# Kernel optimization log

Hardware: AMD Instinct MI355X
Metric: run time of the kernel (lower is better)

Reference implementation:

```python
import jax, jax.numpy as jnp
import numpy as np

IOU_THRESH = 0.5


def _iou_xcycwh(a, b):
    # a: (A,4) center-format anchors, b: (M,4) center-format gt boxes -> (A,M)
    ax1, ay1 = a[:, 0] - a[:, 2] * 0.5, a[:, 1] - a[:, 3] * 0.5
    ax2, ay2 = a[:, 0] + a[:, 2] * 0.5, a[:, 1] + a[:, 3] * 0.5
    bx1, by1 = b[:, 0] - b[:, 2] * 0.5, b[:, 1] - b[:, 3] * 0.5
    bx2, by2 = b[:, 0] + b[:, 2] * 0.5, b[:, 1] + b[:, 3] * 0.5
    iw = jnp.clip(jnp.minimum(ax2[:, None], bx2[None, :]) - jnp.maximum(ax1[:, None], bx1[None, :]), 0.0)
    ih = jnp.clip(jnp.minimum(ay2[:, None], by2[None, :]) - jnp.maximum(ay1[:, None], by1[None, :]), 0.0)
    inter = iw * ih
    area_a = (a[:, 2] * a[:, 3])[:, None]
    area_b = (b[:, 2] * b[:, 3])[None, :]
    return inter / (area_a + area_b - inter)


def _per_image(cls_pred, reg_pred, ann, anchors, num_classes):
    # cls_pred: (A,C) probs in (0,1); reg_pred: (A,5); ann: (M,5) [x,y,w,h,cls]; anchors: (A,4)
    dt = cls_pred.dtype
    valid = ann[:, 4] != -1
    # top-left -> center (matches in-place += w/2, h/2 in torch)
    boxes = jnp.stack([ann[:, 0] + ann[:, 2] * 0.5, ann[:, 1] + ann[:, 3] * 0.5, ann[:, 2], ann[:, 3]], axis=-1)
    ious = _iou_xcycwh(anchors, boxes)                       # (A,M)
    ious = jnp.where(valid[None, :], ious, -jnp.inf)
    ious_max = ious.max(axis=1)
    ious_argmax = ious.argmax(axis=1)
    pos = ious_max >= IOU_THRESH                             # (A,)
    posf = pos.astype(dt)
    npos = pos.sum()
    denom = jnp.maximum(npos, 1).astype(dt)                  # clamp(num_positive_anchors, min=1)
    assigned = jnp.concatenate([boxes, ann[:, 4:5]], axis=-1)[ious_argmax]  # (A,5)
    gt_cls = jax.nn.one_hot(assigned[:, 4].astype(jnp.int32), num_classes, dtype=dt) * posf[:, None]
    bce = -(gt_cls * jnp.log(cls_pred) + (1.0 - gt_cls) * jnp.log(1.0 - cls_pred))
    cls_loss = (bce * posf[:, None]).sum() / denom
    gt_w = jnp.maximum(assigned[:, 2], 1.0)
    gt_h = jnp.maximum(assigned[:, 3], 1.0)
    sig_tx_gt = jax.nn.sigmoid(assigned[:, 0] - anchors[:, 0])
    sig_ty_gt = jax.nn.sigmoid(assigned[:, 1] - anchors[:, 1])
    tw_gt = jnp.log(gt_w / anchors[:, 2])
    th_gt = jnp.log(gt_h / anchors[:, 3])

    def mse(p, t):  # MSELoss over positive anchors = masked sum / npos
        return (posf * (p - t) ** 2).sum() / denom

    reg = (mse(jax.nn.sigmoid(reg_pred[:, 0]), sig_tx_gt)
           + mse(jax.nn.sigmoid(reg_pred[:, 1]), sig_ty_gt)
           + mse(reg_pred[:, 2], tw_gt)
           + mse(reg_pred[:, 3], th_gt)
           + mse(reg_pred[:, 4], jnp.ones_like(reg_pred[:, 4])))
    reg_loss = jnp.where(npos > 0, reg / denom, jnp.zeros((), dt))
    has_valid = valid.any()
    cls_loss = jnp.where(has_valid, cls_loss, jnp.zeros((), dt))
    return cls_loss, reg_loss


def reference(predictions, bbox_annotations, anchors, input_dim, num_classes, num_anchors, grid_size):
    B = predictions.shape[0]
    cls = predictions[..., 5:].reshape(B, -1, num_classes)   # (B,A,C)
    reg = predictions[..., :5].reshape(B, -1, 5)             # (B,A,5)
    anc = anchors.reshape(-1, 4)                             # (A,4)
    cls_l, reg_l = jax.vmap(lambda c, r, a: _per_image(c, r, a, anc, num_classes))(cls, reg, bbox_annotations)
    return cls_l.mean(keepdims=True), reg_l.mean(keepdims=True)


def setup_inputs() -> dict:
    key = jax.random.key(0)
    k1, k2, k3, k4 = jax.random.split(key, 4)
    B, NA, G, C, M, INPUT = 16, 3, 76, 80, 32, 608
    stride = INPUT / G
    # predictions: probabilities/pre-sigmoid values in (0.01, 0.99) (raw log requires p in (0,1))
    u = jax.random.uniform(k1, (B, NA, G, G, C + 5), dtype=jnp.float32)
    predictions = 0.01 + 0.98 * u
    # anchors: grid-cell centers in pixels + 3 per-cell anchor sizes
    xs = (jnp.arange(G, dtype=jnp.float32) + 0.5) * stride
    cyg, cxg = jnp.meshgrid(xs, xs, indexing='ij')
    sizes = jnp.array([[12.0, 16.0], [24.0, 32.0], [48.0, 40.0]], dtype=jnp.float32)
    anchors = jnp.stack([
        jnp.broadcast_to(cxg, (NA, G, G)),
        jnp.broadcast_to(cyg, (NA, G, G)),
        jnp.broadcast_to(sizes[:, 0][:, None, None], (NA, G, G)),
        jnp.broadcast_to(sizes[:, 1][:, None, None], (NA, G, G))], axis=-1)
    # annotations: top-left x,y + w,h in pixels + class id; last 8 boxes padded with cls=-1
    wh = jax.random.uniform(k2, (B, M, 2), minval=8.0, maxval=64.0)
    xy = jax.random.uniform(k3, (B, M, 2), minval=0.0, maxval=INPUT - 64.0)
    cls_id = jax.random.randint(k4, (B, M, 1), 0, C).astype(jnp.float32)
    valid = (jnp.arange(M) < 24)[None, :, None]
    ann = jnp.concatenate([xy, wh, jnp.where(valid, cls_id, -1.0)], axis=-1)
    return {"predictions": predictions, "bbox_annotations": ann, "anchors": anchors,
            "input_dim": INPUT, "num_classes": C, "num_anchors": NA, "grid_size": G}
```

## Files before the change

kernel.cpp:

```cpp
#include <hip/hip_runtime.h>
#include <math.h>


#define NCLS 85
#define CVAL 80
#define BLK  256

__device__ __forceinline__ float sigm(float x) {
    return 1.0f / (1.0f + expf(-x));
}

__global__ void __launch_bounds__(BLK)
yolo_match_kernel(const float* __restrict__ pred,
                  const float* __restrict__ ann,
                  const float* __restrict__ anc,
                  float* __restrict__ partial,
                  int A, int M)
{
    const int b = blockIdx.y;
    const int a = blockIdx.x * BLK + threadIdx.x;

    __shared__ float s_bx1[64], s_by1[64], s_bx2[64], s_by2[64];
    __shared__ float s_bcx[64], s_bcy[64], s_bw[64], s_bh[64], s_area[64];
    __shared__ int   s_cls[64];

    if (threadIdx.x < (unsigned)M) {
        const int m = threadIdx.x;
        const float* r = ann + ((long long)b * M + m) * 5;
        const float x = r[0], y = r[1], w = r[2], h = r[3], c = r[4];
        const float cx = x + 0.5f * w;
        const float cy = y + 0.5f * h;
        s_bcx[m] = cx; s_bcy[m] = cy; s_bw[m] = w; s_bh[m] = h;
        s_bx1[m] = cx - 0.5f * w; s_by1[m] = cy - 0.5f * h;
        s_bx2[m] = cx + 0.5f * w; s_by2[m] = cy + 0.5f * h;
        s_area[m] = w * h;
        s_cls[m] = (c != -1.0f) ? (int)c : -1;
    }
    __syncthreads();

    float cls_sum = 0.0f, reg_sq = 0.0f, np = 0.0f;

    if (a < A) {
        const float4 av = ((const float4*)anc)[a];
        const float acx = av.x, acy = av.y, aw = av.z, ah = av.w;
        const float ax1 = acx - 0.5f * aw, ay1 = acy - 0.5f * ah;
        const float ax2 = acx + 0.5f * aw, ay2 = acy + 0.5f * ah;
        const float aarea = aw * ah;

        float best = -INFINITY;
        int bm = 0;
        for (int m = 0; m < M; ++m) {
            float iw = fminf(ax2, s_bx2[m]) - fmaxf(ax1, s_bx1[m]);
            float ih = fminf(ay2, s_by2[m]) - fmaxf(ay1, s_by1[m]);
            iw = fmaxf(iw, 0.0f);
            ih = fmaxf(ih, 0.0f);
            const float inter = iw * ih;
            float iou = inter / (aarea + s_area[m] - inter);
            if (s_cls[m] < 0) iou = -INFINITY;
            if (iou > best) { best = iou; bm = m; }
        }

        if (best >= 0.5f) {
            np = 1.0f;
            const float bcx = s_bcx[bm], bcy = s_bcy[bm];
            const float bw = s_bw[bm], bh = s_bh[bm];
            const int k = s_cls[bm];

            const float* row = pred + ((long long)b * A + a) * NCLS;

            const float r0 = row[0], r1 = row[1], r2 = row[2], r3 = row[3], r4 = row[4];
            const float e0 = sigm(r0) - sigm(bcx - acx);
            const float e1 = sigm(r1) - sigm(bcy - acy);
            const float e2 = r2 - logf(fmaxf(bw, 1.0f) / aw);
            const float e3 = r3 - logf(fmaxf(bh, 1.0f) / ah);
            const float e4 = r4 - 1.0f;
            reg_sq = e0*e0 + e1*e1 + e2*e2 + e3*e3 + e4*e4;

            for (int c = 0; c < CVAL; ++c) {
                const float p = row[5 + c];
                cls_sum += (c == k) ? -logf(p) : -logf(1.0f - p);
            }
        }
    }

    for (int off = 32; off > 0; off >>= 1) {
        cls_sum += __shfl_down(cls_sum, off);
        reg_sq  += __shfl_down(reg_sq,  off);
        np      += __shfl_down(np,      off);
    }
    __shared__ float s_red[4][3];
    const int wave = threadIdx.x >> 6;
    const int lane = threadIdx.x & 63;
    if (lane == 0) {
        s_red[wave][0] = cls_sum;
        s_red[wave][1] = reg_sq;
        s_red[wave][2] = np;
    }
    __syncthreads();
    if (threadIdx.x == 0) {
        float c = 0.0f, r = 0.0f, n = 0.0f;
        for (int w = 0; w < 4; ++w) { c += s_red[w][0]; r += s_red[w][1]; n += s_red[w][2]; }
        float* dst = partial + ((long long)b * gridDim.x + blockIdx.x) * 3;
        dst[0] = c; dst[1] = r; dst[2] = n;
    }
}

__global__ void __launch_bounds__(256)
yolo_finalize_kernel(const float* __restrict__ partial,
                     float* __restrict__ out, int B, int P)
{
    const int t = threadIdx.x;
    const int b = t >> 4;
    const int j = t & 15;
    float c = 0.0f, r = 0.0f, n = 0.0f;
    if (b < B) {
        for (int p = j; p < P; p += 16) {
            const float* s = partial + ((long long)b * P + p) * 3;
            c += s[0]; r += s[1]; n += s[2];
        }
    }
    for (int m = 8; m > 0; m >>= 1) {
        c += __shfl_xor(c, m);
        r += __shfl_xor(r, m);
        n += __shfl_xor(n, m);
    }
    __shared__ float s_c[16], s_r[16];
    if (j == 0 && b < B) {
        const float denom = fmaxf(n, 1.0f);
        s_c[b] = c / denom;
        s_r[b] = (n > 0.0f) ? r / (denom * denom) : 0.0f;
    }
    __syncthreads();
    if (t == 0) {
        float cs = 0.0f, rs = 0.0f;
        for (int i = 0; i < B; ++i) { cs += s_c[i]; rs += s_r[i]; }
        out[0] = cs / (float)B;
        out[1] = rs / (float)B;
    }
}

extern "C" void kernel_launch(void* const* d_in, const int* in_sizes, int n_in,
                              void* d_out, int out_size, void* d_ws, size_t ws_size,
                              hipStream_t stream) {
    const float* pred = (const float*)d_in[0];
    const float* ann  = (const float*)d_in[1];
    const float* anc  = (const float*)d_in[2];
    float* out = (float*)d_out;

    const int A = in_sizes[2] / 4;
    const int B = in_sizes[0] / (A * NCLS);
    const int M = in_sizes[1] / (5 * B);
    const int P = (A + BLK - 1) / BLK;

    float* partial = (float*)d_ws;

    dim3 grid(P, B);
    yolo_match_kernel<<<grid, dim3(BLK), 0, stream>>>(pred, ann, anc, partial, A, M);
    yolo_finalize_kernel<<<1, 256, 0, stream>>>(partial, out, B, P);
}
```

Baseline: 146.1 us.

## Fuse match and finalize into one cooperative kernel with grid sync

Merges the two kernels into a single cooperative launch that writes per-block partials, performs a grid-wide sync, and lets block (0,0) do the final reduction. Each thread now handles four anchors, which shrinks the grid. Box data is packed into float4 shared arrays, and padded boxes get infinite corners so the per-box validity check drops out of the IoU loop. The intent is to remove one launch and raise per-thread work, at the cost of fewer blocks, a grid sync barrier, and the cooperative-launch limit on co-resident blocks.

```diff
diff --git a/kernel.cpp b/kernel.cpp
--- a/kernel.cpp
+++ b/kernel.cpp
@@ -1,46 +1,62 @@
 #include <hip/hip_runtime.h>
+#include <hip/hip_cooperative_groups.h>
 #include <math.h>
+
+namespace cg = cooperative_groups;
 
 
 #define NCLS 85
 #define CVAL 80
 #define BLK  256
+#define APT  4
 
 __device__ __forceinline__ float sigm(float x) {
     return 1.0f / (1.0f + expf(-x));
 }
 
 __global__ void __launch_bounds__(BLK)
-yolo_match_kernel(const float* __restrict__ pred,
+yolo_fused_kernel(const float* __restrict__ pred,
                   const float* __restrict__ ann,
                   const float* __restrict__ anc,
                   float* __restrict__ partial,
-                  int A, int M)
+                  float* __restrict__ out,
+                  int A, int M, int B, int P)
 {
-    const int b = blockIdx.y;
-    const int a = blockIdx.x * BLK + threadIdx.x;
+    const int b   = blockIdx.y;
+    const int tid = threadIdx.x;
 
-    __shared__ float s_bx1[64], s_by1[64], s_bx2[64], s_by2[64];
-    __shared__ float s_bcx[64], s_bcy[64], s_bw[64], s_bh[64], s_area[64];
-    __shared__ int   s_cls[64];
+    __shared__ float4 s_cor[64];
+    __shared__ float4 s_ctr[64];
+    __shared__ float  s_area[64];
+    __shared__ int    s_cls[64];
 
-    if (threadIdx.x < (unsigned)M) {
-        const int m = threadIdx.x;
+    if (tid < (unsigned)M) {
+        const int m = tid;
         const float* r = ann + ((long long)b * M + m) * 5;
         const float x = r[0], y = r[1], w = r[2], h = r[3], c = r[4];
         const float cx = x + 0.5f * w;
         const float cy = y + 0.5f * h;
-        s_bcx[m] = cx; s_bcy[m] = cy; s_bw[m] = w; s_bh[m] = h;
-        s_bx1[m] = cx - 0.5f * w; s_by1[m] = cy - 0.5f * h;
-        s_bx2[m] = cx + 0.5f * w; s_by2[m] = cy + 0.5f * h;
-        s_area[m] = w * h;
-        s_cls[m] = (c != -1.0f) ? (int)c : -1;
+        const bool valid = (c != -1.0f);
+        if (valid) {
+            s_cor[m] = make_float4(cx - 0.5f * w, cy - 0.5f * h,
+                                   cx + 0.5f * w, cy + 0.5f * h);
+            s_area[m] = w * h;
+        } else {
+            const float inf = INFINITY;
+            s_cor[m] = make_float4(inf, inf, inf, inf);
+            s_area[m] = 0.0f;
+        }
+        s_ctr[m] = make_float4(cx, cy, w, h);
+        s_cls[m] = valid ? (int)c : 0;
     }
     __syncthreads();
 
     float cls_sum = 0.0f, reg_sq = 0.0f, np = 0.0f;
 
-    if (a < A) {
+    for (int k = 0; k < APT; ++k) {
+        const int a = blockIdx.x * (BLK * APT) + k * BLK + tid;
+        if (a >= A) break;
+
         const float4 av = ((const float4*)anc)[a];
         const float acx = av.x, acy = av.y, aw = av.z, ah = av.w;
         const float ax1 = acx - 0.5f * aw, ay1 = acy - 0.5f * ah;
@@ -49,36 +65,35 @@
 
         float best = -INFINITY;
         int bm = 0;
+        #pragma unroll 4
         for (int m = 0; m < M; ++m) {
-            float iw = fminf(ax2, s_bx2[m]) - fmaxf(ax1, s_bx1[m]);
-            float ih = fminf(ay2, s_by2[m]) - fmaxf(ay1, s_by1[m]);
+            const float4 bc = s_cor[m];
+            float iw = fminf(ax2, bc.z) - fmaxf(ax1, bc.x);
+            float ih = fminf(ay2, bc.w) - fmaxf(ay1, bc.y);
             iw = fmaxf(iw, 0.0f);
             ih = fmaxf(ih, 0.0f);
             const float inter = iw * ih;
-            float iou = inter / (aarea + s_area[m] - inter);
-            if (s_cls[m] < 0) iou = -INFINITY;
+            const float iou = inter / (aarea + s_area[m] - inter);
             if (iou > best) { best = iou; bm = m; }
         }
 
         if (best >= 0.5f) {
-            np = 1.0f;
-            const float bcx = s_bcx[bm], bcy = s_bcy[bm];
-            const float bw = s_bw[bm], bh = s_bh[bm];
-            const int k = s_cls[bm];
+            np += 1.0f;
+            const float4 bx = s_ctr[bm];
+            const int kc = s_cls[bm];
 
             const float* row = pred + ((long long)b * A + a) * NCLS;
-
             const float r0 = row[0], r1 = row[1], r2 = row[2], r3 = row[3], r4 = row[4];
-            const float e0 = sigm(r0) - sigm(bcx - acx);
-            const float e1 = sigm(r1) - sigm(bcy - acy);
-            const float e2 = r2 - logf(fmaxf(bw, 1.0f) / aw);
-            const float e3 = r3 - logf(fmaxf(bh, 1.0f) / ah);
+            const float e0 = sigm(r0) - sigm(bx.x - acx);
+            const float e1 = sigm(r1) - sigm(bx.y - acy);
+            const float e2 = r2 - logf(fmaxf(bx.z, 1.0f) / aw);
+            const float e3 = r3 - logf(fmaxf(bx.w, 1.0f) / ah);
             const float e4 = r4 - 1.0f;
-            reg_sq = e0*e0 + e1*e1 + e2*e2 + e3*e3 + e4*e4;
+            reg_sq += e0*e0 + e1*e1 + e2*e2 + e3*e3 + e4*e4;
 
             for (int c = 0; c < CVAL; ++c) {
                 const float p = row[5 + c];
-                cls_sum += (c == k) ? -logf(p) : -logf(1.0f - p);
+                cls_sum += (c == kc) ? -logf(p) : -logf(1.0f - p);
             }
         }
     }
@@ -89,53 +104,51 @@
         np      += __shfl_down(np,      off);
     }
     __shared__ float s_red[4][3];
-    const int wave = threadIdx.x >> 6;
-    const int lane = threadIdx.x & 63;
+    const int wave = tid >> 6;
+    const int lane = tid & 63;
     if (lane == 0) {
         s_red[wave][0] = cls_sum;
         s_red[wave][1] = reg_sq;
         s_red[wave][2] = np;
     }
     __syncthreads();
-    if (threadIdx.x == 0) {
+    if (tid == 0) {
         float c = 0.0f, r = 0.0f, n = 0.0f;
         for (int w = 0; w < 4; ++w) { c += s_red[w][0]; r += s_red[w][1]; n += s_red[w][2]; }
-        float* dst = partial + ((long long)b * gridDim.x + blockIdx.x) * 3;
+        float* dst = partial + ((long long)b * P + blockIdx.x) * 3;
         dst[0] = c; dst[1] = r; dst[2] = n;
     }
-}
 
-__global__ void __launch_bounds__(256)
-yolo_finalize_kernel(const float* __restrict__ partial,
-                     float* __restrict__ out, int B, int P)
-{
-    const int t = threadIdx.x;
-    const int b = t >> 4;
-    const int j = t & 15;
-    float c = 0.0f, r = 0.0f, n = 0.0f;
-    if (b < B) {
-        for (int p = j; p < P; p += 16) {
-            const float* s = partial + ((long long)b * P + p) * 3;
-            c += s[0]; r += s[1]; n += s[2];
+    cg::this_grid().sync();
+
+    if (blockIdx.x == 0 && blockIdx.y == 0) {
+        const int bi = tid >> 4;
+        const int j  = tid & 15;
+        float c = 0.0f, r = 0.0f, n = 0.0f;
+        if (bi < B) {
+            for (int p = j; p < P; p += 16) {
+                const float* s = partial + ((long long)bi * P + p) * 3;
+                c += s[0]; r += s[1]; n += s[2];
+            }
         }
-    }
-    for (int m = 8; m > 0; m >>= 1) {
-        c += __shfl_xor(c, m);
-        r += __shfl_xor(r, m);
-        n += __shfl_xor(n, m);
-    }
-    __shared__ float s_c[16], s_r[16];
-    if (j == 0 && b < B) {
-        const float denom = fmaxf(n, 1.0f);
-        s_c[b] = c / denom;
-        s_r[b] = (n > 0.0f) ? r / (denom * denom) : 0.0f;
-    }
-    __syncthreads();
-    if (t == 0) {
-        float cs = 0.0f, rs = 0.0f;
-        for (int i = 0; i < B; ++i) { cs += s_c[i]; rs += s_r[i]; }
-        out[0] = cs / (float)B;
-        out[1] = rs / (float)B;
+        for (int m = 8; m > 0; m >>= 1) {
+            c += __shfl_xor(c, m);
+            r += __shfl_xor(r, m);
+            n += __shfl_xor(n, m);
+        }
+        __shared__ float f_c[16], f_r[16];
+        if (j == 0 && bi < B) {
+            const float denom = fmaxf(n, 1.0f);
+            f_c[bi] = c / denom;
+            f_r[bi] = (n > 0.0f) ? r / (denom * denom) : 0.0f;
+        }
+        __syncthreads();
+        if (tid == 0) {
+            float cs = 0.0f, rs = 0.0f;
+            for (int i = 0; i < B; ++i) { cs += f_c[i]; rs += f_r[i]; }
+            out[0] = cs / (float)B;
+            out[1] = rs / (float)B;
+        }
     }
 }
 
@@ -147,14 +160,15 @@
     const float* anc  = (const float*)d_in[2];
     float* out = (float*)d_out;
 
-    const int A = in_sizes[2] / 4;
-    const int B = in_sizes[0] / (A * NCLS);
-    const int M = in_sizes[1] / (5 * B);
-    const int P = (A + BLK - 1) / BLK;
+    int A = in_sizes[2] / 4;
+    int B = in_sizes[0] / (A * NCLS);
+    int M = in_sizes[1] / (5 * B);
+    int P = (A + BLK * APT - 1) / (BLK * APT);
 
     float* partial = (float*)d_ws;
 
-    dim3 grid(P, B);
-    yolo_match_kernel<<<grid, dim3(BLK), 0, stream>>>(pred, ann, anc, partial, A, M);
-    yolo_finalize_kernel<<<1, 256, 0, stream>>>(partial, out, B, P);
+    void* args[] = { (void*)&pred, (void*)&ann, (void*)&anc, (void*)&partial,
+                     (void*)&out, (void*)&A, (void*)&M, (void*)&B, (void*)&P };
+    hipLaunchCooperativeKernel((const void*)yolo_fused_kernel,
+                               dim3(P, B), dim3(BLK), args, 0, stream);
 }
```

After: 197.1 us. 34.9% more time.
